# Optimization experiments

Hardware: AMD Instinct MI355X
Metric: run time of the kernel (lower is better)

## Reference

```python
import jax, jax.numpy as jnp
import numpy as np

TEMPERATURE = 0.5
EPSILON = 1e-08
NEG_POS_RATIO = 4
B = 4096          # per-view batch
D = 512           # embedding dim
N = 2 * B         # total rows in sim matrix


def setup_inputs() -> dict:
    key = jax.random.key(0)
    k1, k2, k3 = jax.random.split(key, 3)
    z_i = jax.random.normal(k1, (B, D), dtype=jnp.float32)
    z_j = jax.random.normal(k2, (B, D), dtype=jnp.float32)
    # torch.multinomial over uniform ones, with replacement, over the 2B-1
    # non-diagonal columns == uniform randint in [0, N-1).
    neg_idx = jax.random.randint(k3, (N, NEG_POS_RATIO), 0, N - 1, dtype=jnp.int32)
    return {"z_i": z_i, "z_j": z_j, "neg_idx": neg_idx}


def reference(z_i, z_j, neg_idx):
    z = jnp.concatenate((z_i, z_j), axis=0)                      # [N, D]
    # cosine similarity matrix via normalize + matmul (same math as
    # F.cosine_similarity(z[:,None], z[None,:], dim=2), eps=1e-8 default)
    zn = z / jnp.maximum(jnp.linalg.norm(z, axis=1, keepdims=True), 1e-8)
    sim = (zn @ zn.T) / (TEMPERATURE + EPSILON)                  # [N, N]

    rows = jnp.arange(N)
    positives = sim[rows, (rows + B) % N]                        # [N]

    # negatives_all[i] = sim[i] with column i removed; sampled index k in
    # [0, N-1) maps to original column k if k < i else k + 1.
    cols = neg_idx + (neg_idx >= rows[:, None]).astype(neg_idx.dtype)  # [N, R]
    negatives = jnp.take_along_axis(sim, cols, axis=1)           # [N, R]

    logits = jnp.concatenate((positives[:, None], negatives), axis=1)  # [N, 1+R]
    nll = -jax.nn.log_softmax(logits, axis=1)[:, 0]              # labels all 0
    # weighted CE with weight[0]=neg_pos_ratio; all labels are 0 so the
    # per-sample weight cancels in the mean reduction:
    # loss = sum(w0 * nll) / sum(w0) = mean(nll)
    w0 = jnp.float32(NEG_POS_RATIO)
    loss = (w0 * nll).sum() / (w0 * N)
    return loss
```

## Files before the change

### kernel.cpp

```cpp
#include <hip/hip_runtime.h>
#include <math.h>

#define B_ROWS 4096
#define D_DIM  512
#define N_ROWS 8192
#define R_NEG  4

__device__ const float INV_T = (float)(1.0 / (0.5 + 1e-8));

__global__ __launch_bounds__(256) void norms_kernel(
    const float* __restrict__ zi, const float* __restrict__ zj,
    float* __restrict__ inv_norm) {
  int wave = threadIdx.x >> 6;
  int lane = threadIdx.x & 63;
  int row  = blockIdx.x * 4 + wave;
  if (row >= N_ROWS) return;
  const float* z = (row < B_ROWS) ? (zi + (size_t)row * D_DIM)
                                  : (zj + (size_t)(row - B_ROWS) * D_DIM);
  const float4* z4 = (const float4*)z;
  float4 a = z4[lane];
  float4 b = z4[lane + 64];
  float s = a.x * a.x + a.y * a.y + a.z * a.z + a.w * a.w +
            b.x * b.x + b.y * b.y + b.z * b.z + b.w * b.w;
#pragma unroll
  for (int off = 32; off > 0; off >>= 1) s += __shfl_down(s, off);
  if (lane == 0) {
    inv_norm[row] = 1.0f / fmaxf(sqrtf(s), 1e-8f);
  }
}

__global__ __launch_bounds__(256) void loss_kernel(
    const float* __restrict__ zi, const float* __restrict__ zj,
    const int* __restrict__ neg_idx, const float* __restrict__ inv_norm,
    float* __restrict__ nll_out) {
  int wave = threadIdx.x >> 6;
  int lane = threadIdx.x & 63;
  int row  = blockIdx.x * 4 + wave;
  if (row >= N_ROWS) return;

  const float4* a4 =
      (row < B_ROWS) ? (const float4*)(zi + (size_t)row * D_DIM)
                     : (const float4*)(zj + (size_t)(row - B_ROWS) * D_DIM);
  float4 a0 = a4[lane];
  float4 a1 = a4[lane + 64];

  int cols[5];
  cols[0] = (row + B_ROWS) % N_ROWS;
#pragma unroll
  for (int r = 0; r < R_NEG; ++r) {
    int k = neg_idx[row * R_NEG + r];
    cols[r + 1] = k + (k >= row ? 1 : 0);
  }

  float logits[5];
#pragma unroll
  for (int c = 0; c < 5; ++c) {
    int col = cols[c];
    const float4* b4 =
        (col < B_ROWS) ? (const float4*)(zi + (size_t)col * D_DIM)
                       : (const float4*)(zj + (size_t)(col - B_ROWS) * D_DIM);
    float4 b0 = b4[lane];
    float4 b1 = b4[lane + 64];
    float s = a0.x * b0.x + a0.y * b0.y + a0.z * b0.z + a0.w * b0.w +
              a1.x * b1.x + a1.y * b1.y + a1.z * b1.z + a1.w * b1.w;
#pragma unroll
    for (int off = 32; off > 0; off >>= 1) s += __shfl_down(s, off);
    logits[c] = s;
  }

  if (lane == 0) {
    float inv_i = inv_norm[row];
    float m = -INFINITY;
#pragma unroll
    for (int c = 0; c < 5; ++c) {
      logits[c] *= inv_i * inv_norm[cols[c]] * INV_T;
      m = fmaxf(m, logits[c]);
    }
    float sum = 0.0f;
#pragma unroll
    for (int c = 0; c < 5; ++c) sum += __expf(logits[c] - m);
    float nll = -(logits[0] - m - __logf(sum));
    nll_out[row] = nll;
  }
}

__global__ __launch_bounds__(256) void reduce_kernel(
    const float* __restrict__ nll, float* __restrict__ out) {
  __shared__ float smem[4];
  int lane = threadIdx.x & 63;
  int wave = threadIdx.x >> 6;
  float s = 0.0f;
  for (int i = threadIdx.x; i < N_ROWS; i += 256) s += nll[i];
#pragma unroll
  for (int off = 32; off > 0; off >>= 1) s += __shfl_down(s, off);
  if (lane == 0) smem[wave] = s;
  __syncthreads();
  if (threadIdx.x == 0) {
    float t = smem[0] + smem[1] + smem[2] + smem[3];
    out[0] = t * (1.0f / (float)N_ROWS);
  }
}

extern "C" void kernel_launch(void* const* d_in, const int* in_sizes, int n_in,
                              void* d_out, int out_size, void* d_ws,
                              size_t ws_size, hipStream_t stream) {
  const float* zi      = (const float*)d_in[0];
  const float* zj      = (const float*)d_in[1];
  const int*   neg_idx = (const int*)d_in[2];
  float* out = (float*)d_out;

  float* inv_norm = (float*)d_ws;
  float* nll      = inv_norm + N_ROWS;

  dim3 block(256);
  dim3 grid(N_ROWS / 4);

  norms_kernel<<<grid, block, 0, stream>>>(zi, zj, inv_norm);
  loss_kernel<<<grid, block, 0, stream>>>(zi, zj, neg_idx, inv_norm, nll);
  reduce_kernel<<<1, block, 0, stream>>>(nll, out);
}
```

Baseline: 87.28 us.

## Fuse norm, loss and reduction into one kernel with last-block reduce

Merges the three kernels into a single kernel. Each wave now computes the row and gathered-column norms inline, alongside the dot products, instead of reading precomputed inverse norms. The final mean is done by the last block to finish, detected with an atomic counter that is reset by a memset before launch. The aim is to cut launch overhead and the separate full pass over the embeddings for norms, at the cost of extra per-row norm work, more registers for the five prefetched column vectors, and a memset call.

```diff
diff --git a/kernel.cpp b/kernel.cpp
--- a/kernel.cpp
+++ b/kernel.cpp
@@ -5,38 +5,33 @@
 #define D_DIM  512
 #define N_ROWS 8192
 #define R_NEG  4
+#define NBLOCKS (N_ROWS / 4)
 
-__device__ const float INV_T = (float)(1.0 / (0.5 + 1e-8));
+#define INV_T 2.0f
 
-__global__ __launch_bounds__(256) void norms_kernel(
-    const float* __restrict__ zi, const float* __restrict__ zj,
-    float* __restrict__ inv_norm) {
-  int wave = threadIdx.x >> 6;
-  int lane = threadIdx.x & 63;
-  int row  = blockIdx.x * 4 + wave;
-  if (row >= N_ROWS) return;
-  const float* z = (row < B_ROWS) ? (zi + (size_t)row * D_DIM)
-                                  : (zj + (size_t)(row - B_ROWS) * D_DIM);
-  const float4* z4 = (const float4*)z;
-  float4 a = z4[lane];
-  float4 b = z4[lane + 64];
-  float s = a.x * a.x + a.y * a.y + a.z * a.z + a.w * a.w +
-            b.x * b.x + b.y * b.y + b.z * b.z + b.w * b.w;
-#pragma unroll
-  for (int off = 32; off > 0; off >>= 1) s += __shfl_down(s, off);
-  if (lane == 0) {
-    inv_norm[row] = 1.0f / fmaxf(sqrtf(s), 1e-8f);
-  }
+__device__ __forceinline__ float dot4(float4 a, float4 b) {
+  return a.x * b.x + a.y * b.y + a.z * b.z + a.w * b.w;
 }
 
-__global__ __launch_bounds__(256) void loss_kernel(
+__global__ __launch_bounds__(256) void fused_loss_kernel(
     const float* __restrict__ zi, const float* __restrict__ zj,
-    const int* __restrict__ neg_idx, const float* __restrict__ inv_norm,
-    float* __restrict__ nll_out) {
-  int wave = threadIdx.x >> 6;
-  int lane = threadIdx.x & 63;
-  int row  = blockIdx.x * 4 + wave;
-  if (row >= N_ROWS) return;
+    const int* __restrict__ neg_idx, float* __restrict__ partials,
+    int* __restrict__ counter, float* __restrict__ out) {
+  __shared__ float s_nll[4];
+  __shared__ int s_last;
+  __shared__ float s_fin[4];
+
+  const int wave = threadIdx.x >> 6;
+  const int lane = threadIdx.x & 63;
+  const int row  = blockIdx.x * 4 + wave;
+
+  const int4 nv = ((const int4*)neg_idx)[row];
+  int cols[5];
+  cols[0] = (row + B_ROWS) & (N_ROWS - 1);
+  cols[1] = nv.x + (nv.x >= row ? 1 : 0);
+  cols[2] = nv.y + (nv.y >= row ? 1 : 0);
+  cols[3] = nv.z + (nv.z >= row ? 1 : 0);
+  cols[4] = nv.w + (nv.w >= row ? 1 : 0);
 
   const float4* a4 =
       (row < B_ROWS) ? (const float4*)(zi + (size_t)row * D_DIM)
@@ -44,60 +39,72 @@
   float4 a0 = a4[lane];
   float4 a1 = a4[lane + 64];
 
-  int cols[5];
-  cols[0] = (row + B_ROWS) % N_ROWS;
-#pragma unroll
-  for (int r = 0; r < R_NEG; ++r) {
-    int k = neg_idx[row * R_NEG + r];
-    cols[r + 1] = k + (k >= row ? 1 : 0);
-  }
-
-  float logits[5];
+  float4 b0[5], b1[5];
 #pragma unroll
   for (int c = 0; c < 5; ++c) {
-    int col = cols[c];
+    const int col = cols[c];
     const float4* b4 =
         (col < B_ROWS) ? (const float4*)(zi + (size_t)col * D_DIM)
                        : (const float4*)(zj + (size_t)(col - B_ROWS) * D_DIM);
-    float4 b0 = b4[lane];
-    float4 b1 = b4[lane + 64];
-    float s = a0.x * b0.x + a0.y * b0.y + a0.z * b0.z + a0.w * b0.w +
-              a1.x * b1.x + a1.y * b1.y + a1.z * b1.z + a1.w * b1.w;
+    b0[c] = b4[lane];
+    b1[c] = b4[lane + 64];
+  }
+
+  float aa = dot4(a0, a0) + dot4(a1, a1);
+  float ab[5], bb[5];
 #pragma unroll
-    for (int off = 32; off > 0; off >>= 1) s += __shfl_down(s, off);
-    logits[c] = s;
+  for (int c = 0; c < 5; ++c) {
+    ab[c] = dot4(a0, b0[c]) + dot4(a1, b1[c]);
+    bb[c] = dot4(b0[c], b0[c]) + dot4(b1[c], b1[c]);
+  }
+
+#pragma unroll
+  for (int off = 32; off > 0; off >>= 1) {
+    aa += __shfl_down(aa, off);
+#pragma unroll
+    for (int c = 0; c < 5; ++c) {
+      ab[c] += __shfl_down(ab[c], off);
+      bb[c] += __shfl_down(bb[c], off);
+    }
   }
 
   if (lane == 0) {
-    float inv_i = inv_norm[row];
+    const float inv_a = 1.0f / fmaxf(sqrtf(aa), 1e-8f);
+    float logits[5];
     float m = -INFINITY;
 #pragma unroll
     for (int c = 0; c < 5; ++c) {
-      logits[c] *= inv_i * inv_norm[cols[c]] * INV_T;
+      const float inv_b = 1.0f / fmaxf(sqrtf(bb[c]), 1e-8f);
+      logits[c] = ab[c] * inv_a * inv_b * INV_T;
       m = fmaxf(m, logits[c]);
     }
     float sum = 0.0f;
 #pragma unroll
     for (int c = 0; c < 5; ++c) sum += __expf(logits[c] - m);
-    float nll = -(logits[0] - m - __logf(sum));
-    nll_out[row] = nll;
+    s_nll[wave] = -(logits[0] - m - __logf(sum));
   }
-}
+  __syncthreads();
 
-__global__ __launch_bounds__(256) void reduce_kernel(
-    const float* __restrict__ nll, float* __restrict__ out) {
-  __shared__ float smem[4];
-  int lane = threadIdx.x & 63;
-  int wave = threadIdx.x >> 6;
-  float s = 0.0f;
-  for (int i = threadIdx.x; i < N_ROWS; i += 256) s += nll[i];
+  if (threadIdx.x == 0) {
+    partials[blockIdx.x] = s_nll[0] + s_nll[1] + s_nll[2] + s_nll[3];
+    __threadfence();
+    int old = atomicAdd(counter, 1);
+    s_last = (old == NBLOCKS - 1) ? 1 : 0;
+  }
+  __syncthreads();
+
+  if (s_last) {
+    __threadfence();
+    float s = 0.0f;
+    for (int i = threadIdx.x; i < NBLOCKS; i += 256) s += partials[i];
 #pragma unroll
-  for (int off = 32; off > 0; off >>= 1) s += __shfl_down(s, off);
-  if (lane == 0) smem[wave] = s;
-  __syncthreads();
-  if (threadIdx.x == 0) {
-    float t = smem[0] + smem[1] + smem[2] + smem[3];
-    out[0] = t * (1.0f / (float)N_ROWS);
+    for (int off = 32; off > 0; off >>= 1) s += __shfl_down(s, off);
+    if (lane == 0) s_fin[wave] = s;
+    __syncthreads();
+    if (threadIdx.x == 0) {
+      out[0] = (s_fin[0] + s_fin[1] + s_fin[2] + s_fin[3]) *
+               (1.0f / (float)N_ROWS);
+    }
   }
 }
 
@@ -109,13 +116,11 @@
   const int*   neg_idx = (const int*)d_in[2];
   float* out = (float*)d_out;
 
-  float* inv_norm = (float*)d_ws;
-  float* nll      = inv_norm + N_ROWS;
+  float* partials = (float*)d_ws;
+  int*   counter  = (int*)((char*)d_ws + NBLOCKS * sizeof(float));
 
-  dim3 block(256);
-  dim3 grid(N_ROWS / 4);
+  hipMemsetAsync(counter, 0, sizeof(int), stream);
 
-  norms_kernel<<<grid, block, 0, stream>>>(zi, zj, inv_norm);
-  loss_kernel<<<grid, block, 0, stream>>>(zi, zj, neg_idx, inv_norm, nll);
-  reduce_kernel<<<1, block, 0, stream>>>(nll, out);
+  fused_loss_kernel<<<dim3(NBLOCKS), dim3(256), 0, stream>>>(
+      zi, zj, neg_idx, partials, counter, out);
 }
```

After: 141.8 us. +62.4%, slower.
